# Kernel tuning notes

Hardware: AMD Instinct MI355X
Metric: run time of the kernel (lower is better)

Reference implementation:

```python
import jax, jax.numpy as jnp
import numpy as np

NUM_HEADS = 16
HIDDEN = 1024
HEAD_DIM = HIDDEN // NUM_HEADS


def setup_inputs() -> dict:
    key = jax.random.key(0)
    ks = jax.random.split(key, 12)
    B, S, H = 4, 1024, HIDDEN
    s = 1.0 / np.sqrt(H)
    inp = {
        "aspect_hidden": jax.random.normal(ks[0], (B, S, H), jnp.float32),
        "opinion_hidden": jax.random.normal(ks[1], (B, S, H), jnp.float32),
        "attention_mask": jnp.ones((B, S), jnp.int32),
        # torch nn.Linear weights are [out, in]
        "Wq": jax.random.normal(ks[2], (H, H), jnp.float32) * s,
        "bq": jnp.zeros((H,), jnp.float32),
        "Wk": jax.random.normal(ks[3], (H, H), jnp.float32) * s,
        "bk": jnp.zeros((H,), jnp.float32),
        "Wv": jax.random.normal(ks[4], (H, H), jnp.float32) * s,
        "bv": jnp.zeros((H,), jnp.float32),
        "Wo": jax.random.normal(ks[5], (H, H), jnp.float32) * s,
        "bo": jnp.zeros((H,), jnp.float32),
        # nn.Bilinear(H, H, 1): weight [1, H, H], bias [1]
        "Wbil": jax.random.normal(ks[6], (1, H, H), jnp.float32) * s,
        "bbil": jnp.zeros((1,), jnp.float32),
    }
    return inp


def reference(aspect_hidden, opinion_hidden, attention_mask,
              Wq, bq, Wk, bk, Wv, bv, Wo, bo, Wbil, bbil):
    B, Sq, H = aspect_hidden.shape
    Sk = opinion_hidden.shape[1]
    nh, hd = NUM_HEADS, HEAD_DIM
    scale = hd ** (-0.5)

    q = (aspect_hidden @ Wq.T + bq).reshape(B, Sq, nh, hd).transpose(0, 2, 1, 3)
    k = (opinion_hidden @ Wk.T + bk).reshape(B, Sk, nh, hd).transpose(0, 2, 1, 3)
    v = (opinion_hidden @ Wv.T + bv).reshape(B, Sk, nh, hd).transpose(0, 2, 1, 3)

    # bilinear span bias: span[b,s] = a[b,s] @ Wbil[0] @ o[b,s] + bbil
    span = jnp.einsum('bsh,hk,bsk->bs', aspect_hidden, Wbil[0], opinion_hidden) + bbil[0]

    # scores [B, nh, Sq, Sk] with span bias broadcast over heads and keys
    scores = jnp.einsum('bhqd,bhkd->bhqk', q, k) * scale + span[:, None, :, None]
    scores = jnp.where(attention_mask[:, None, None, :] == 0, -jnp.inf, scores)

    probs = jax.nn.softmax(scores, axis=-1)
    ctx = jnp.einsum('bhqk,bhkd->bhqd', probs, v)
    ctx = ctx.transpose(0, 2, 1, 3).reshape(B, Sq, H)
    return ctx @ Wo.T + bo
```

## Files before the change

kernel.cpp:

```cpp
#include <hip/hip_runtime.h>
#include <hip/hip_bf16.h>
#include <stdint.h>

typedef __attribute__((ext_vector_type(4))) float f32x4;
typedef __attribute__((ext_vector_type(16))) float f32x16;
typedef __attribute__((ext_vector_type(8))) short bf16x8;
typedef __attribute__((ext_vector_type(4))) unsigned int u32x4;
typedef __attribute__((ext_vector_type(2))) unsigned int u32x2;
typedef unsigned short u16;

#define GBL_AS1(p) ((const __attribute__((address_space(1))) void*)(p))
#define LDS_AS3(p) ((__attribute__((address_space(3))) void*)(p))

static __device__ __forceinline__ u16 f2bf(float f) {
  __hip_bfloat16 h = __float2bfloat16(f);
  union { __hip_bfloat16 h; u16 u; } c; c.h = h;
  return c.u;
}

__global__ __launch_bounds__(256) void fused_cast(
    const float* __restrict__ a, const float* __restrict__ o,
    const float* __restrict__ wq_, const float* __restrict__ wk_,
    const float* __restrict__ wv_, const float* __restrict__ wo_,
    const int* __restrict__ mask,
    u16* __restrict__ aB, u16* __restrict__ oB,
    u16* __restrict__ WqB, u16* __restrict__ WkB,
    u16* __restrict__ WvB, u16* __restrict__ WoB,
    int* __restrict__ flags) {
  if (blockIdx.x == 0 && threadIdx.x < 64) {
    int bb = threadIdx.x >> 4, kt = threadIdx.x & 15;
    int anyz = 0;
    for (int s = 0; s < 64; ++s) anyz |= (mask[bb * 1024 + kt * 64 + s] == 0);
    flags[threadIdx.x] = anyz;
  }
  int idx = blockIdx.x * 256 + threadIdx.x;
#pragma unroll
  for (int j = 0; j < 4; ++j) {
    int i = idx + j * 786432;
    const float* src; u16* dst; int off;
    if (i < 1048576) { src = a; dst = aB; off = i; }
    else if (i < 2097152) { src = o; dst = oB; off = i - 1048576; }
    else {
      int w = (i - 2097152) >> 18; off = (i - 2097152) & 262143;
      src = (w == 0) ? wq_ : (w == 1) ? wk_ : (w == 2) ? wv_ : wo_;
      dst = (w == 0) ? WqB : (w == 1) ? WkB : (w == 2) ? WvB : WoB;
    }
    float4 v = reinterpret_cast<const float4*>(src)[off];
    ushort4 ov;
    ov.x = f2bf(v.x); ov.y = f2bf(v.y); ov.z = f2bf(v.z); ov.w = f2bf(v.w);
    reinterpret_cast<ushort4*>(dst)[off] = ov;
  }
}

static __device__ __forceinline__ void gemm_core(const u16* __restrict__ Atile,
                                                 const u16* __restrict__ Btile,
                                                 u16* lds_a, u16* lds_b,
                                                 f32x4 acc[4][4]) {
  const int tid = threadIdx.x;
  const int lane = tid & 63;
  const int wv = tid >> 6;
  const int wm = wv >> 1, wn = wv & 1;
  const int fr = lane & 15, fq = lane >> 4;

#define GSTAGE(kt_, buf_) do { \
    _Pragma("unroll") \
    for (int i_ = 0; i_ < 2; ++i_) { \
      const int cb_ = (wv * 2 + i_) * 64; \
      const int c_ = cb_ + lane; \
      const int row_ = c_ >> 2; \
      const int off_ = (c_ & 3) * 8; \
      __builtin_amdgcn_global_load_lds(GBL_AS1(Atile + (size_t)row_ * 1024 + (kt_) * 32 + off_), \
                                       LDS_AS3(lds_a + (buf_) * 4096 + cb_ * 8), 16, 0, 0); \
      __builtin_amdgcn_global_load_lds(GBL_AS1(Btile + (size_t)row_ * 1024 + (kt_) * 32 + off_), \
                                       LDS_AS3(lds_b + (buf_) * 4096 + cb_ * 8), 16, 0, 0); \
    } \
  } while (0)

  GSTAGE(0, 0);
  __syncthreads();
  for (int kt = 0; kt < 32; ++kt) {
    const int cur = kt & 1;
    if (kt < 31) GSTAGE(kt + 1, cur ^ 1);
    const u16* la = lds_a + cur * 4096;
    const u16* lb = lds_b + cur * 4096;
    bf16x8 af[4], bfv[4];
#pragma unroll
    for (int mi = 0; mi < 4; ++mi)
      af[mi] = *(const bf16x8*)&la[(wm * 64 + mi * 16 + fr) * 32 + fq * 8];
#pragma unroll
    for (int ni = 0; ni < 4; ++ni)
      bfv[ni] = *(const bf16x8*)&lb[(wn * 64 + ni * 16 + fr) * 32 + fq * 8];
#pragma unroll
    for (int mi = 0; mi < 4; ++mi)
#pragma unroll
      for (int ni = 0; ni < 4; ++ni)
        acc[mi][ni] = __builtin_amdgcn_mfma_f32_16x16x32_bf16(af[mi], bfv[ni], acc[mi][ni], 0, 0, 0);
    __syncthreads();
  }
#undef GSTAGE
}

__global__ __launch_bounds__(256) void qkv_gemm(
    const u16* __restrict__ aB, const u16* __restrict__ oB,
    const u16* __restrict__ Wq, const u16* __restrict__ Wk, const u16* __restrict__ Wv,
    const float* __restrict__ bq, const float* __restrict__ bk, const float* __restrict__ bv,
    u16* __restrict__ q_ws, u16* __restrict__ k_ws, u16* __restrict__ vt_ws) {
  __shared__ __align__(16) u16 lds_a[2 * 128 * 32];
  __shared__ __align__(16) u16 lds_b[2 * 128 * 32];
  const int bid = blockIdx.x;
  const int wk = (bid & 7) * 96 + (bid >> 3);
  const int mt = wk & 31, nt = wk >> 5;
  const int w = nt >> 3, ntl = nt & 7;
  const u16* A = (w == 0) ? aB : oB;
  const u16* W = (w == 0) ? Wq : (w == 1) ? Wk : Wv;
  const float* bias = (w == 0) ? bq : (w == 1) ? bk : bv;
  f32x4 acc[4][4];
#pragma unroll
  for (int i = 0; i < 4; ++i)
#pragma unroll
    for (int j = 0; j < 4; ++j) acc[i][j] = (f32x4){0.f, 0.f, 0.f, 0.f};
  gemm_core(A + (size_t)mt * 128 * 1024, W + (size_t)ntl * 128 * 1024, lds_a, lds_b, acc);
  const int lane = threadIdx.x & 63, wvi = threadIdx.x >> 6;
  const int wm = wvi >> 1, wn = wvi & 1, fr = lane & 15, fq = lane >> 4;
  if (w < 2) {
    u16* dst01 = (w == 0) ? q_ws : k_ws;
    const float qscl = (w == 0) ? 0.18033688f : 1.0f;
#pragma unroll
    for (int mi = 0; mi < 4; ++mi)
#pragma unroll
      for (int ni = 0; ni < 4; ++ni)
#pragma unroll
        for (int r = 0; r < 4; ++r) {
          int m = mt * 128 + wm * 64 + mi * 16 + fq * 4 + r;
          int nl = ntl * 128 + wn * 64 + ni * 16 + fr;
          float v = (acc[mi][ni][r] + bias[nl]) * qscl;
          int b = m >> 10, s = m & 1023, h = nl >> 6, d = nl & 63;
          dst01[(((size_t)(b * 16 + h)) * 1024 + s) * 64 + d] = f2bf(v);
        }
  } else {
#pragma unroll
    for (int mi = 0; mi < 4; ++mi)
#pragma unroll
      for (int ni = 0; ni < 4; ++ni) {
        int nl = ntl * 128 + wn * 64 + ni * 16 + fr;
        int h = nl >> 6, d = nl & 63;
        float bv_ = bias[nl];
        int m0 = mt * 128 + wm * 64 + mi * 16 + fq * 4;
        int b = m0 >> 10, s0 = m0 & 1023;
        ushort4 o;
        o.x = f2bf(acc[mi][ni][0] + bv_);
        o.y = f2bf(acc[mi][ni][1] + bv_);
        o.z = f2bf(acc[mi][ni][2] + bv_);
        o.w = f2bf(acc[mi][ni][3] + bv_);
        *(ushort4*)&vt_ws[(((size_t)(b * 16 + h)) * 64 + d) * 1024 + s0] = o;
      }
  }
}

__global__ __launch_bounds__(256, 4) void attn_kernel(
    const u16* __restrict__ q_ws, const u16* __restrict__ k_ws,
    const u16* __restrict__ vt_ws, const int* __restrict__ mask,
    const int* __restrict__ flags, u16* __restrict__ ctx_ws) {
  __shared__ __align__(16) u16 k_lds[2][64 * 64];
  __shared__ __align__(16) u16 vt_lds[2][64 * 64];
  __shared__ __align__(16) float scl_lds[4][32];
  const int bid = blockIdx.x;
  const int bh = bid & 63, qt = bid >> 6;
  const int b = bh >> 4, h = bh & 15;
  const int tid = threadIdx.x, lane = tid & 63, wv = tid >> 6;
  const int l31 = lane & 31, hi = lane >> 5;
  const u16* qbase = q_ws + (size_t)bh * 65536 + (size_t)qt * 8192;
  const u16* kbase = k_ws + (size_t)bh * 65536;
  const u16* vtbase = vt_ws + (size_t)bh * 65536;

#define STAGE_KV(kt_, buf_) do { \
    _Pragma("unroll") \
    for (int i_ = 0; i_ < 2; ++i_) { \
      int cb_ = (wv * 2 + i_) * 64; \
      int c_ = cb_ + lane; \
      int r_ = c_ >> 3; \
      int sc_ = ((c_ & 7) ^ (r_ & 7)) * 8; \
      __builtin_amdgcn_global_load_lds(GBL_AS1(kbase + (size_t)((kt_) * 64 + r_) * 64 + sc_), \
                                       LDS_AS3(&k_lds[buf_][cb_ * 8]), 16, 0, 0); \
      __builtin_amdgcn_global_load_lds(GBL_AS1(vtbase + (size_t)r_ * 1024 + (kt_) * 64 + sc_), \
                                       LDS_AS3(&vt_lds[buf_][cb_ * 8]), 16, 0, 0); \
    } \
  } while (0)

  {
    u16* qstage = &k_lds[0][0];
#pragma unroll
    for (int i_ = 0; i_ < 4; ++i_) {
      int cb_ = (wv * 4 + i_) * 64;
      int c_ = cb_ + lane;
      int r_ = c_ >> 3;
      int sc_ = ((c_ & 7) ^ (r_ & 7)) * 8;
      __builtin_amdgcn_global_load_lds(GBL_AS1(qbase + (size_t)r_ * 64 + sc_),
                                       LDS_AS3(qstage + cb_ * 8), 16, 0, 0);
    }
  }
  __syncthreads();
  bf16x8 qf[4];
  {
    int rq = wv * 32 + l31;
    const u16* qr = &k_lds[0][0] + rq * 64;
    int rx = rq & 7;
#pragma unroll
    for (int ds = 0; ds < 4; ++ds)
      qf[ds] = *(const bf16x8*)&qr[((ds * 2 + hi) ^ rx) * 8];
  }
  __syncthreads();
  STAGE_KV(0, 0);
  __syncthreads();

  f32x16 ctx0, ctx1;
#pragma unroll
  for (int z = 0; z < 16; ++z) { ctx0[z] = 0.f; ctx1[z] = 0.f; }
  float psum_half = 0.f;

  for (int kt = 0; kt < 16; ++kt) {
    const int cur = kt & 1;
    if (kt < 15) STAGE_KV(kt + 1, cur ^ 1);

    f32x16 sc[2];
#pragma unroll
    for (int kb = 0; kb < 2; ++kb) {
      f32x16 a;
#pragma unroll
      for (int z = 0; z < 16; ++z) a[z] = 0.f;
      int r = kb * 32 + l31;
      const u16* kr = &k_lds[cur][r * 64];
      int rx = r & 7;
#pragma unroll
      for (int ds = 0; ds < 4; ++ds) {
        bf16x8 kf = *(const bf16x8*)&kr[((ds * 2 + hi) ^ rx) * 8];
        a = __builtin_amdgcn_mfma_f32_32x32x16_bf16(kf, qf[ds], a, 0, 0, 0);
      }
      sc[kb] = a;
    }

    if (flags[b * 16 + kt]) {
#pragma unroll
      for (int kb = 0; kb < 2; ++kb)
#pragma unroll
        for (int r2 = 0; r2 < 16; ++r2) {
          int key = kb * 32 + (r2 & 3) + 8 * (r2 >> 2) + 4 * hi;
          if (mask[b * 1024 + kt * 64 + key] == 0) sc[kb][r2] = -30000.0f;
        }
    }

#pragma unroll
    for (int kb = 0; kb < 2; ++kb)
#pragma unroll
      for (int r2 = 0; r2 < 16; ++r2) {
        float p = __builtin_exp2f(sc[kb][r2]);
        sc[kb][r2] = p;
        psum_half += p;
      }

#pragma unroll
    for (int kb = 0; kb < 2; ++kb) {
      unsigned int w[8];
#pragma unroll
      for (int j = 0; j < 8; ++j) {
        unsigned int t;
        asm("v_cvt_pk_bf16_f32 %0, %1, %2" : "=v"(t) : "v"(sc[kb][2 * j]), "v"(sc[kb][2 * j + 1]));
        w[j] = t;
      }
      u32x2 a0 = __builtin_amdgcn_permlane32_swap(w[0], w[2], false, false);
      u32x2 a1 = __builtin_amdgcn_permlane32_swap(w[1], w[3], false, false);
      u32x2 a2 = __builtin_amdgcn_permlane32_swap(w[4], w[6], false, false);
      u32x2 a3 = __builtin_amdgcn_permlane32_swap(w[5], w[7], false, false);
      union { u32x4 u; bf16x8 b; } P0, P1;
      P0.u = (u32x4){ a0[0], a1[0], a0[1], a1[1] };
      P1.u = (u32x4){ a2[0], a3[0], a2[1], a3[1] };
#pragma unroll
      for (int db = 0; db < 2; ++db) {
        int rv = db * 32 + l31;
        const u16* vr = &vt_lds[cur][rv * 64];
        int rvx = rv & 7;
        bf16x8 v0 = *(const bf16x8*)&vr[((kb * 4 + hi) ^ rvx) * 8];
        bf16x8 v1 = *(const bf16x8*)&vr[((kb * 4 + 2 + hi) ^ rvx) * 8];
        if (db == 0) {
          ctx0 = __builtin_amdgcn_mfma_f32_32x32x16_bf16(P0.b, v0, ctx0, 0, 0, 0);
          ctx0 = __builtin_amdgcn_mfma_f32_32x32x16_bf16(P1.b, v1, ctx0, 0, 0, 0);
        } else {
          ctx1 = __builtin_amdgcn_mfma_f32_32x32x16_bf16(P0.b, v0, ctx1, 0, 0, 0);
          ctx1 = __builtin_amdgcn_mfma_f32_32x32x16_bf16(P1.b, v1, ctx1, 0, 0, 0);
        }
      }
    }
    __syncthreads();
  }

  float lrow = psum_half + __shfl_xor(psum_half, 32);
  float inv = (lrow > 0.f) ? 1.0f / lrow : 0.f;
  if (hi == 0) scl_lds[wv][l31] = inv;
  asm volatile("s_waitcnt lgkmcnt(0)" ::: "memory");
  const int sbase = qt * 128 + wv * 32;
#pragma unroll
  for (int g = 0; g < 4; ++g) {
    float4 s4 = *(const float4*)&scl_lds[wv][g * 8 + hi * 4];
    const float* sp = (const float*)&s4;
#pragma unroll
    for (int i2 = 0; i2 < 4; ++i2) {
      int s = sbase + g * 8 + hi * 4 + i2;
      size_t rowoff = ((size_t)(b * 1024 + s)) * 1024 + h * 64;
      ctx_ws[rowoff + l31]      = f2bf(ctx0[g * 4 + i2] * sp[i2]);
      ctx_ws[rowoff + 32 + l31] = f2bf(ctx1[g * 4 + i2] * sp[i2]);
    }
  }
#undef STAGE_KV
}

__global__ __launch_bounds__(256) void out_gemm(const u16* __restrict__ ctxB,
                                                const u16* __restrict__ Wo,
                                                const float* __restrict__ bo,
                                                float* __restrict__ out) {
  __shared__ __align__(16) u16 lds_a[2 * 128 * 32];
  __shared__ __align__(16) u16 lds_b[2 * 128 * 32];
  const int bid = blockIdx.x;
  const int wk = (bid & 7) * 32 + (bid >> 3);
  const int mt = wk & 31, nt = wk >> 5;
  f32x4 acc[4][4];
#pragma unroll
  for (int i = 0; i < 4; ++i)
#pragma unroll
    for (int j = 0; j < 4; ++j) acc[i][j] = (f32x4){0.f, 0.f, 0.f, 0.f};
  gemm_core(ctxB + (size_t)mt * 128 * 1024, Wo + (size_t)nt * 128 * 1024, lds_a, lds_b, acc);
  const int lane = threadIdx.x & 63, wvi = threadIdx.x >> 6;
  const int wm = wvi >> 1, wn = wvi & 1, fr = lane & 15, fq = lane >> 4;
#pragma unroll
  for (int mi = 0; mi < 4; ++mi)
#pragma unroll
    for (int ni = 0; ni < 4; ++ni)
#pragma unroll
      for (int r = 0; r < 4; ++r) {
        int m = mt * 128 + wm * 64 + mi * 16 + fq * 4 + r;
        int n = nt * 128 + wn * 64 + ni * 16 + fr;
        out[(size_t)m * 1024 + n] = acc[mi][ni][r] + bo[n];
      }
}

extern "C" void kernel_launch(void* const* d_in, const int* in_sizes, int n_in,
                              void* d_out, int out_size, void* d_ws, size_t ws_size,
                              hipStream_t stream) {
  const float* aspect = (const float*)d_in[0];
  const float* opinion = (const float*)d_in[1];
  const int* mask = (const int*)d_in[2];
  const float* Wq = (const float*)d_in[3];
  const float* bq = (const float*)d_in[4];
  const float* Wk = (const float*)d_in[5];
  const float* bk = (const float*)d_in[6];
  const float* Wv = (const float*)d_in[7];
  const float* bv = (const float*)d_in[8];
  const float* Wo = (const float*)d_in[9];
  const float* bo = (const float*)d_in[10];
  float* out = (float*)d_out;
  char* ws = (char*)d_ws;

  const size_t MB = 1u << 20;
  u16* aB    = (u16*)(ws + 0 * MB);
  u16* oB    = (u16*)(ws + 8 * MB);
  u16* WqB   = (u16*)(ws + 16 * MB);
  u16* WkB   = (u16*)(ws + 18 * MB);
  u16* WvB   = (u16*)(ws + 20 * MB);
  u16* WoB   = (u16*)(ws + 22 * MB);
  u16* q_ws  = (u16*)(ws + 24 * MB);
  u16* k_ws  = (u16*)(ws + 32 * MB);
  u16* vt_ws = (u16*)(ws + 40 * MB);
  u16* ctx_ws= (u16*)(ws + 48 * MB);
  int* flags = (int*)(out + out_size - 64);

  fused_cast<<<3072, 256, 0, stream>>>(aspect, opinion, Wq, Wk, Wv, Wo, mask,
                                       aB, oB, WqB, WkB, WvB, WoB, flags);
  qkv_gemm<<<768, 256, 0, stream>>>(aB, oB, WqB, WkB, WvB, bq, bk, bv,
                                    q_ws, k_ws, vt_ws);
  attn_kernel<<<512, 256, 0, stream>>>(q_ws, k_ws, vt_ws, mask, flags, ctx_ws);
  out_gemm<<<256, 256, 0, stream>>>(ctx_ws, WoB, bo, out);
}
```

Baseline: 130.5 us.

## Triple-buffer GEMM LDS staging with explicit vmcnt waits and 2D grids

The shared GEMM core moves from a double-buffered to a triple-buffered LDS pipeline that prefetches two k-tiles ahead. It replaces __syncthreads with explicit s_waitcnt vmcnt counts plus raw barriers, so global loads can stay in flight across iterations. The QKV and output GEMMs also drop the XCD-aware block swizzle in favour of a plain 2D grid. This costs more LDS per block, and the blocks no longer map onto XCDs in a way that favours L2 reuse.

```diff
diff --git a/kernel.cpp b/kernel.cpp
--- a/kernel.cpp
+++ b/kernel.cpp
@@ -52,10 +52,10 @@
   }
 }
 
-static __device__ __forceinline__ void gemm_core(const u16* __restrict__ Atile,
-                                                 const u16* __restrict__ Btile,
-                                                 u16* lds_a, u16* lds_b,
-                                                 f32x4 acc[4][4]) {
+static __device__ __forceinline__ void gemm_core3(const u16* __restrict__ Atile,
+                                                  const u16* __restrict__ Btile,
+                                                  u16* lds_a, u16* lds_b,
+                                                  f32x4 acc[4][4]) {
   const int tid = threadIdx.x;
   const int lane = tid & 63;
   const int wv = tid >> 6;
@@ -77,10 +77,20 @@
   } while (0)
 
   GSTAGE(0, 0);
-  __syncthreads();
+  GSTAGE(1, 1);
+  int cur = 0;
   for (int kt = 0; kt < 32; ++kt) {
-    const int cur = kt & 1;
-    if (kt < 31) GSTAGE(kt + 1, cur ^ 1);
+    if (kt < 30) {
+      int nxt = cur + 2; if (nxt >= 3) nxt -= 3;
+      GSTAGE(kt + 2, nxt);
+      asm volatile("s_waitcnt vmcnt(8)" ::: "memory");
+    } else if (kt == 30) {
+      asm volatile("s_waitcnt vmcnt(4)" ::: "memory");
+    } else {
+      asm volatile("s_waitcnt vmcnt(0)" ::: "memory");
+    }
+    __builtin_amdgcn_s_barrier();
+    __builtin_amdgcn_sched_barrier(0);
     const u16* la = lds_a + cur * 4096;
     const u16* lb = lds_b + cur * 4096;
     bf16x8 af[4], bfv[4];
@@ -95,7 +105,9 @@
 #pragma unroll
       for (int ni = 0; ni < 4; ++ni)
         acc[mi][ni] = __builtin_amdgcn_mfma_f32_16x16x32_bf16(af[mi], bfv[ni], acc[mi][ni], 0, 0, 0);
-    __syncthreads();
+    __builtin_amdgcn_sched_barrier(0);
+    __builtin_amdgcn_s_barrier();
+    cur = (cur + 1 == 3) ? 0 : cur + 1;
   }
 #undef GSTAGE
 }
@@ -105,11 +117,10 @@
     const u16* __restrict__ Wq, const u16* __restrict__ Wk, const u16* __restrict__ Wv,
     const float* __restrict__ bq, const float* __restrict__ bk, const float* __restrict__ bv,
     u16* __restrict__ q_ws, u16* __restrict__ k_ws, u16* __restrict__ vt_ws) {
-  __shared__ __align__(16) u16 lds_a[2 * 128 * 32];
-  __shared__ __align__(16) u16 lds_b[2 * 128 * 32];
-  const int bid = blockIdx.x;
-  const int wk = (bid & 7) * 96 + (bid >> 3);
-  const int mt = wk & 31, nt = wk >> 5;
+  __shared__ __align__(16) u16 lds_a[3 * 128 * 32];
+  __shared__ __align__(16) u16 lds_b[3 * 128 * 32];
+  const int mt = blockIdx.x;
+  const int nt = blockIdx.y;
   const int w = nt >> 3, ntl = nt & 7;
   const u16* A = (w == 0) ? aB : oB;
   const u16* W = (w == 0) ? Wq : (w == 1) ? Wk : Wv;
@@ -119,7 +130,7 @@
   for (int i = 0; i < 4; ++i)
 #pragma unroll
     for (int j = 0; j < 4; ++j) acc[i][j] = (f32x4){0.f, 0.f, 0.f, 0.f};
-  gemm_core(A + (size_t)mt * 128 * 1024, W + (size_t)ntl * 128 * 1024, lds_a, lds_b, acc);
+  gemm_core3(A + (size_t)mt * 128 * 1024, W + (size_t)ntl * 128 * 1024, lds_a, lds_b, acc);
   const int lane = threadIdx.x & 63, wvi = threadIdx.x >> 6;
   const int wm = wvi >> 1, wn = wvi & 1, fr = lane & 15, fq = lane >> 4;
   if (w < 2) {
@@ -317,17 +328,15 @@
                                                 const u16* __restrict__ Wo,
                                                 const float* __restrict__ bo,
                                                 float* __restrict__ out) {
-  __shared__ __align__(16) u16 lds_a[2 * 128 * 32];
-  __shared__ __align__(16) u16 lds_b[2 * 128 * 32];
-  const int bid = blockIdx.x;
-  const int wk = (bid & 7) * 32 + (bid >> 3);
-  const int mt = wk & 31, nt = wk >> 5;
+  __shared__ __align__(16) u16 lds_a[3 * 128 * 32];
+  __shared__ __align__(16) u16 lds_b[3 * 128 * 32];
+  const int mt = blockIdx.x, nt = blockIdx.y;
   f32x4 acc[4][4];
 #pragma unroll
   for (int i = 0; i < 4; ++i)
 #pragma unroll
     for (int j = 0; j < 4; ++j) acc[i][j] = (f32x4){0.f, 0.f, 0.f, 0.f};
-  gemm_core(ctxB + (size_t)mt * 128 * 1024, Wo + (size_t)nt * 128 * 1024, lds_a, lds_b, acc);
+  gemm_core3(ctxB + (size_t)mt * 128 * 1024, Wo + (size_t)nt * 128 * 1024, lds_a, lds_b, acc);
   const int lane = threadIdx.x & 63, wvi = threadIdx.x >> 6;
   const int wm = wvi >> 1, wn = wvi & 1, fr = lane & 15, fq = lane >> 4;
 #pragma unroll
@@ -374,8 +383,8 @@
 
   fused_cast<<<3072, 256, 0, stream>>>(aspect, opinion, Wq, Wk, Wv, Wo, mask,
                                        aB, oB, WqB, WkB, WvB, WoB, flags);
-  qkv_gemm<<<768, 256, 0, stream>>>(aB, oB, WqB, WkB, WvB, bq, bk, bv,
-                                    q_ws, k_ws, vt_ws);
+  qkv_gemm<<<dim3(32, 24), 256, 0, stream>>>(aB, oB, WqB, WkB, WvB, bq, bk, bv,
+                                             q_ws, k_ws, vt_ws);
   attn_kernel<<<512, 256, 0, stream>>>(q_ws, k_ws, vt_ws, mask, flags, ctx_ws);
-  out_gemm<<<256, 256, 0, stream>>>(ctx_ws, WoB, bo, out);
-}
+  out_gemm<<<dim3(32, 8), 256, 0, stream>>>(ctx_ws, WoB, bo, out);
+}
```

After: 120.3 us. -7.9%, faster.
